# Kernel optimization log

Hardware: AMD Instinct MI355X
Metric: run time of the kernel (lower is better)

## Reference

```python
import jax, jax.numpy as jnp
import numpy as np

B, S, E = 2, 2048, 1024
H, KVH, D = 16, 4, 64
ROPE_BASE = 10000.0


def setup_inputs() -> dict:
    key = jax.random.key(0)
    ks = jax.random.split(key, 7)
    s = 0.02
    return {
        "query_inputs": jax.random.normal(ks[0], (B, S, E), jnp.float32),
        "key_inputs": jax.random.normal(ks[1], (B, S, E), jnp.float32),
        "value_inputs": jax.random.normal(ks[2], (B, S, E), jnp.float32),
        "attention_mask": jnp.ones((1, 1, S, S), dtype=bool),
        "Wq": jax.random.normal(ks[3], (E, H * D), jnp.float32) * s,
        "Wk": jax.random.normal(ks[4], (E, KVH * D), jnp.float32) * s,
        "Wv": jax.random.normal(ks[5], (E, KVH * D), jnp.float32) * s,
        "Wo": jax.random.normal(ks[6], (H * D, E), jnp.float32) * s,
    }


def _rotate_half(x):
    x1, x2 = jnp.split(x, 2, axis=-1)
    return jnp.concatenate((-x2, x1), axis=-1)


def _rope(k, q):
    # standard RoPE, rescaling_factor=None -> base 10000
    d = q.shape[-1]
    inv_freq = 1.0 / (ROPE_BASE ** (jnp.arange(0, d, 2, dtype=jnp.float32) / d))
    t = jnp.arange(q.shape[1], dtype=jnp.float32)
    freqs = jnp.einsum("i,j->ij", t, inv_freq)          # [S, d/2]
    emb = jnp.concatenate((freqs, freqs), axis=-1)       # [S, d]
    cos = jnp.cos(emb)[None, :, None, :]                 # [1, S, 1, d]
    sin = jnp.sin(emb)[None, :, None, :]
    apply = lambda x: x * cos + _rotate_half(x) * sin
    return apply(k), apply(q)


def reference(query_inputs, key_inputs, value_inputs, attention_mask, Wq, Wk, Wv, Wo):
    q = (query_inputs @ Wq).reshape(B, S, H, D)
    k = (key_inputs @ Wk).reshape(B, S, KVH, D)
    v = (value_inputs @ Wv).reshape(B, S, KVH, D)
    k, q = _rope(k, q)
    n_rep = H // KVH
    k = jnp.repeat(k, n_rep, axis=2)                     # [B, S, H, D]
    v = jnp.repeat(v, n_rep, axis=2)
    logits = jnp.einsum("bthd,bThd->bhtT", q, k) / jnp.sqrt(jnp.float32(D))
    logits = jnp.where(attention_mask, logits, jnp.float32(-1e30))
    w = jax.nn.softmax(logits, axis=-1)                  # [B, H, S, S]
    out = jnp.einsum("bhtT,bThd->bthd", w, v).reshape(B, S, H * D)
    return out @ Wo
```

## Files before the change

### kernel.cpp

```cpp
#include <hip/hip_runtime.h>
#include <hip/hip_bf16.h>
#include <math.h>

#define Bsz 2
#define Sseq 2048
#define Edim 1024
#define Hq 16
#define KVH 4
#define Dh 64

typedef __attribute__((ext_vector_type(2))) float f32x2;
typedef __attribute__((ext_vector_type(4))) float f32x4;
typedef __attribute__((ext_vector_type(16))) float f32x16;
typedef __attribute__((ext_vector_type(8))) short bf16x8;

__device__ inline unsigned short f2bf(float f) {
    union { float f; unsigned int u; } v; v.f = f;
    unsigned int u = v.u;
    u += 0x7FFFu + ((u >> 16) & 1u);
    return (unsigned short)(u >> 16);
}

__device__ inline float bf2f(unsigned short u) {
    union { unsigned int u; float f; } v; v.u = (unsigned int)u << 16;
    return v.f;
}

__device__ inline unsigned int cvt_pk_bf16(float a, float b) {
    unsigned int r;
    asm("v_cvt_pk_bf16_f32 %0, %1, %2" : "=v"(r) : "v"(a), "v"(b));
    return r;
}

__device__ inline f32x4 mfma16(bf16x8 a, bf16x8 b, f32x4 c) {
    return __builtin_amdgcn_mfma_f32_16x16x32_bf16(a, b, c, 0, 0, 0);
}

__device__ inline f32x16 mfma32(bf16x8 a, bf16x8 b, f32x16 c) {
    return __builtin_amdgcn_mfma_f32_32x32x16_bf16(a, b, c, 0, 0, 0);
}

__device__ inline void gload_lds16(const void* g, void* l) {
    __builtin_amdgcn_global_load_lds(
        (const __attribute__((address_space(1))) unsigned int*)g,
        (__attribute__((address_space(3))) unsigned int*)l, 16, 0, 0);
}

__global__ __launch_bounds__(256)
void prep(const float* __restrict__ Xq, const float* __restrict__ Xk,
          const float* __restrict__ Xv,
          const float* __restrict__ Wq, const float* __restrict__ Wk,
          const float* __restrict__ Wv, const float* __restrict__ Wo,
          unsigned short* __restrict__ Xq_b, unsigned short* __restrict__ Xk_b,
          unsigned short* __restrict__ Xv_b,
          unsigned short* __restrict__ Wq_t, unsigned short* __restrict__ Wk_t,
          unsigned short* __restrict__ Wv_t, unsigned short* __restrict__ Wo_t,
          float* __restrict__ tab) {
    int bid = blockIdx.x;
    if (bid < 256) {
        int idx = bid * 256 + threadIdx.x;
        int s = idx >> 5, j = idx & 31;
        double inv = pow(10000.0, -(double)(2 * j) / 64.0);
        double a = (double)s * inv;
        tab[idx * 2 + 0] = (float)cos(a);
        tab[idx * 2 + 1] = (float)sin(a);
        return;
    }
    bid -= 256;
    if (bid < 12288) {
        const float* X; unsigned short* Y;
        if (bid < 4096)      { X = Xq; Y = Xq_b; }
        else if (bid < 8192) { X = Xk; Y = Xk_b; bid -= 4096; }
        else                 { X = Xv; Y = Xv_b; bid -= 8192; }
        int i = bid * 256 + threadIdx.x;
        float4 v = ((const float4*)X)[i];
        ushort4 o;
        o.x = f2bf(v.x); o.y = f2bf(v.y); o.z = f2bf(v.z); o.w = f2bf(v.w);
        ((ushort4*)Y)[i] = o;
        return;
    }
    bid -= 12288;
    const float* W; unsigned short* Wt; int N; int local;
    if (bid < 1024)      { W = Wq; Wt = Wq_t; N = 1024; local = bid; }
    else if (bid < 1280) { W = Wk; Wt = Wk_t; N = 256;  local = bid - 1024; }
    else if (bid < 1536) { W = Wv; Wt = Wv_t; N = 256;  local = bid - 1280; }
    else                 { W = Wo; Wt = Wo_t; N = 1024; local = bid - 1536; }
    __shared__ float tile[32][33];
    int nb = N >> 5;
    int bn = (local % nb) * 32, bk = (local / nb) * 32;
    int tx = threadIdx.x & 31, ty = threadIdx.x >> 5;
    #pragma unroll
    for (int i = 0; i < 32; i += 8)
        tile[ty + i][tx] = W[(size_t)(bk + ty + i) * N + bn + tx];
    __syncthreads();
    #pragma unroll
    for (int i = 0; i < 32; i += 8)
        Wt[(size_t)(bn + ty + i) * 1024 + bk + tx] = f2bf(tile[tx][ty + i]);
}

__global__ __launch_bounds__(256)
void qkv_gemm(const unsigned short* __restrict__ Xq_b,
              const unsigned short* __restrict__ Xk_b,
              const unsigned short* __restrict__ Xv_b,
              const unsigned short* __restrict__ Wq_t,
              const unsigned short* __restrict__ Wk_t,
              const unsigned short* __restrict__ Wv_t,
              unsigned short* __restrict__ Qb,
              unsigned short* __restrict__ Kbf,
              unsigned short* __restrict__ Vt,
              const float* __restrict__ tab, float qscale) {
    __shared__ __attribute__((aligned(16))) unsigned short Alds[128 * 64];
    __shared__ __attribute__((aligned(16))) unsigned short Blds[64 * 64];

    int bid = blockIdx.x;
    const unsigned short *A, *Bt;
    unsigned short* C;
    int m0, n0, N, epi;
    float prescale;
    if (bid < 512) {
        A = Xq_b; Bt = Wq_t; C = Qb;
        m0 = (bid & 31) << 7; n0 = (bid >> 5) << 6; N = 1024; epi = 0; prescale = qscale;
    } else if (bid < 640) {
        int l = bid - 512;
        A = Xk_b; Bt = Wk_t; C = Kbf;
        m0 = (l & 31) << 7; n0 = (l >> 5) << 6; N = 256; epi = 0; prescale = 1.f;
    } else {
        int l = bid - 640;
        A = Xv_b; Bt = Wv_t; C = Vt;
        m0 = (l & 31) << 7; n0 = (l >> 5) << 6; N = 256; epi = 1; prescale = 1.f;
    }

    const int t = threadIdx.x;
    const int wid = t >> 6, lane = t & 63;
    const int l15 = lane & 15, l4 = lane >> 4;
    const int wm = wid * 32;

    f32x4 acc[2][4] = {};

    for (int k0 = 0; k0 < 1024; k0 += 64) {
        #pragma unroll
        for (int i = 0; i < 4; ++i) {
            int slot = t + 256 * i;
            int row = slot >> 3, ch = slot & 7;
            int g = ch ^ (row & 7);
            gload_lds16(A + (size_t)(m0 + row) * 1024 + k0 + g * 8, &Alds[slot * 8]);
        }
        #pragma unroll
        for (int i = 0; i < 2; ++i) {
            int slot = t + 256 * i;
            int row = slot >> 3, ch = slot & 7;
            int g = ch ^ (row & 7);
            gload_lds16(Bt + (size_t)(n0 + row) * 1024 + k0 + g * 8, &Blds[slot * 8]);
        }
        __syncthreads();
        __builtin_amdgcn_s_setprio(1);
        #pragma unroll
        for (int kc = 0; kc < 2; ++kc) {
            bf16x8 af[2], bfr[4];
            #pragma unroll
            for (int mt = 0; mt < 2; ++mt)
                af[mt] = *(const bf16x8*)&Alds[(wm + mt * 16 + l15) * 64 + (((kc * 4 + l4) ^ (l15 & 7)) * 8)];
            #pragma unroll
            for (int nt = 0; nt < 4; ++nt)
                bfr[nt] = *(const bf16x8*)&Blds[(nt * 16 + l15) * 64 + (((kc * 4 + l4) ^ (l15 & 7)) * 8)];
            #pragma unroll
            for (int mt = 0; mt < 2; ++mt)
                #pragma unroll
                for (int nt = 0; nt < 4; ++nt)
                    acc[mt][nt] = mfma16(af[mt], bfr[nt], acc[mt][nt]);
        }
        __builtin_amdgcn_s_setprio(0);
        __syncthreads();
    }

    if (epi == 0) {
        #pragma unroll
        for (int mt = 0; mt < 2; ++mt) {
            int rbase = m0 + wm + mt * 16 + 4 * l4;
            #pragma unroll
            for (int nt = 0; nt < 2; ++nt) {
                int col = n0 + nt * 16 + l15;
                int j = col & 31;
                #pragma unroll
                for (int r = 0; r < 4; ++r) {
                    int row = rbase + r;
                    int s = row & (Sseq - 1);
                    float c = tab[(s * 32 + j) * 2 + 0];
                    float sn = tab[(s * 32 + j) * 2 + 1];
                    float x1 = acc[mt][nt][r] * prescale;
                    float x2 = acc[mt][nt + 2][r] * prescale;
                    C[(size_t)row * N + col]      = f2bf(x1 * c - x2 * sn);
                    C[(size_t)row * N + col + 32] = f2bf(x2 * c + x1 * sn);
                }
            }
        }
    } else {
        #pragma unroll
        for (int mt = 0; mt < 2; ++mt)
            #pragma unroll
            for (int nt = 0; nt < 4; ++nt)
                #pragma unroll
                for (int r = 0; r < 4; ++r) {
                    int row = m0 + wm + mt * 16 + 4 * l4 + r;
                    int col = n0 + nt * 16 + l15;
                    int b = row >> 11, s = row & (Sseq - 1);
                    C[((size_t)(b * 256 + col) << 11) + s] = f2bf(acc[mt][nt][r]);
                }
    }
}

__global__ __launch_bounds__(256)
void wo_gemm(const unsigned short* __restrict__ A,
             const unsigned short* __restrict__ Bt,
             float* __restrict__ C) {
    __shared__ __attribute__((aligned(16))) unsigned short Alds[128 * 64];
    __shared__ __attribute__((aligned(16))) unsigned short Blds[64 * 64];
    const int t = threadIdx.x;
    const int wid = t >> 6, lane = t & 63;
    const int l15 = lane & 15, l4 = lane >> 4;
    const int m0 = blockIdx.x * 128, n0 = blockIdx.y * 64;
    const int wm = wid * 32;

    f32x4 acc[2][4] = {};

    for (int k0 = 0; k0 < 1024; k0 += 64) {
        #pragma unroll
        for (int i = 0; i < 4; ++i) {
            int slot = t + 256 * i;
            int row = slot >> 3, ch = slot & 7;
            int g = ch ^ (row & 7);
            gload_lds16(A + (size_t)(m0 + row) * 1024 + k0 + g * 8, &Alds[slot * 8]);
        }
        #pragma unroll
        for (int i = 0; i < 2; ++i) {
            int slot = t + 256 * i;
            int row = slot >> 3, ch = slot & 7;
            int g = ch ^ (row & 7);
            gload_lds16(Bt + (size_t)(n0 + row) * 1024 + k0 + g * 8, &Blds[slot * 8]);
        }
        __syncthreads();
        __builtin_amdgcn_s_setprio(1);
        #pragma unroll
        for (int kc = 0; kc < 2; ++kc) {
            bf16x8 af[2], bfr[4];
            #pragma unroll
            for (int mt = 0; mt < 2; ++mt)
                af[mt] = *(const bf16x8*)&Alds[(wm + mt * 16 + l15) * 64 + (((kc * 4 + l4) ^ (l15 & 7)) * 8)];
            #pragma unroll
            for (int nt = 0; nt < 4; ++nt)
                bfr[nt] = *(const bf16x8*)&Blds[(nt * 16 + l15) * 64 + (((kc * 4 + l4) ^ (l15 & 7)) * 8)];
            #pragma unroll
            for (int mt = 0; mt < 2; ++mt)
                #pragma unroll
                for (int nt = 0; nt < 4; ++nt)
                    acc[mt][nt] = mfma16(af[mt], bfr[nt], acc[mt][nt]);
        }
        __builtin_amdgcn_s_setprio(0);
        __syncthreads();
    }

    #pragma unroll
    for (int mt = 0; mt < 2; ++mt)
        #pragma unroll
        for (int nt = 0; nt < 4; ++nt)
            #pragma unroll
            for (int r = 0; r < 4; ++r)
                C[(size_t)(m0 + wm + mt * 16 + 4 * l4 + r) * 1024 + n0 + nt * 16 + l15]
                    = acc[mt][nt][r];
}

__global__ __launch_bounds__(256, 4)
void attn_split(const unsigned short* __restrict__ Q,
                const unsigned short* __restrict__ Kb,
                const unsigned short* __restrict__ Vt,
                unsigned short* __restrict__ Op,
                float* __restrict__ Lp) {
    __shared__ __attribute__((aligned(16))) unsigned short Klds[2][64 * 64];
    __shared__ __attribute__((aligned(16))) unsigned short Vlds[2][64 * 64];

    const int t = threadIdx.x, wid = t >> 6, lane = t & 63;
    const int l31 = lane & 31, hi = lane >> 5;
    const int q0 = blockIdx.x * 128;
    const int bh = blockIdx.y;
    const int half = blockIdx.z;
    const int b = bh >> 4, h = bh & 15, kvh = h >> 2;
    const int qb0 = (b << 11) + q0 + wid * 32;
    const int kh0 = half * 1024;

    bf16x8 qf[4];
    {
        const unsigned short* qp = Q + (size_t)(qb0 + l31) * 1024 + h * 64 + hi * 8;
        #pragma unroll
        for (int kc = 0; kc < 4; ++kc)
            qf[kc] = *(const bf16x8*)(qp + kc * 16);
    }

    const int r0 = t >> 3, c0 = t & 7;
    const int g0 = c0 ^ (r0 & 7);
    const int r1 = r0 + 32;
    const int g1 = c0 ^ (r1 & 7);
    const unsigned short* kp0 = Kb + (((size_t)((b << 11) + kh0 + r0)) << 8) + kvh * 64 + g0 * 8;
    const unsigned short* kp1 = Kb + (((size_t)((b << 11) + kh0 + r1)) << 8) + kvh * 64 + g1 * 8;
    const unsigned short* vp0 = Vt + (((size_t)((b * 4 + kvh) * 64 + r0)) << 11) + kh0 + g0 * 8;
    const unsigned short* vp1 = Vt + (((size_t)((b * 4 + kvh) * 64 + r1)) << 11) + kh0 + g1 * 8;

    f32x16 accO[2] = {};
    float lrow = 0.f;

    #define STAGE(buf)                                                    \
        do {                                                              \
            gload_lds16(kp0, &Klds[buf][t * 8]);                          \
            gload_lds16(kp1, &Klds[buf][(t + 256) * 8]);                  \
            gload_lds16(vp0, &Vlds[buf][t * 8]);                          \
            gload_lds16(vp1, &Vlds[buf][(t + 256) * 8]);                  \
            kp0 += 64 * 256; kp1 += 64 * 256; vp0 += 64; vp1 += 64;       \
        } while (0)

    STAGE(0);
    asm volatile("s_waitcnt vmcnt(0)");
    __syncthreads();

    int cur = 0;
    for (int kt = 0; kt < 16; ++kt) {
        if (kt + 1 < 16) STAGE(cur ^ 1);

        f32x16 sacc[2] = {};
        __builtin_amdgcn_s_setprio(1);
        #pragma unroll
        for (int kc = 0; kc < 4; ++kc) {
            #pragma unroll
            for (int kb = 0; kb < 2; ++kb) {
                int row = kb * 32 + l31;
                bf16x8 kf = *(const bf16x8*)
                    &Klds[cur][row * 64 + (((kc * 2 + hi) ^ (row & 7)) * 8)];
                sacc[kb] = mfma32(kf, qf[kc], sacc[kb]);
            }
        }
        __builtin_amdgcn_s_setprio(0);

        float pv[2][16];
        f32x2 rs2 = {0.f, 0.f};
        #pragma unroll
        for (int kb = 0; kb < 2; ++kb)
            #pragma unroll
            for (int r = 0; r < 16; r += 2) {
                float p0 = __builtin_amdgcn_exp2f(sacc[kb][r]);
                float p1 = __builtin_amdgcn_exp2f(sacc[kb][r + 1]);
                pv[kb][r] = p0;
                pv[kb][r + 1] = p1;
                rs2 += (f32x2){p0, p1};
            }
        float rs = rs2[0] + rs2[1];
        lrow += rs + __shfl_xor(rs, 32);

        bf16x8 pa[4];
        #pragma unroll
        for (int kb = 0; kb < 2; ++kb) {
            #pragma unroll
            for (int hf = 0; hf < 2; ++hf) {
                const float* p = &pv[kb][hf * 8];
                unsigned int u0 = cvt_pk_bf16(p[0], p[1]);
                unsigned int u1 = cvt_pk_bf16(p[2], p[3]);
                unsigned int u2 = cvt_pk_bf16(p[4], p[5]);
                unsigned int u3 = cvt_pk_bf16(p[6], p[7]);
                asm("v_permlane32_swap_b32 %0, %1" : "+v"(u0), "+v"(u2));
                asm("v_permlane32_swap_b32 %0, %1" : "+v"(u1), "+v"(u3));
                uint4 w; w.x = u0; w.y = u1; w.z = u2; w.w = u3;
                pa[kb * 2 + hf] = *(bf16x8*)&w;
            }
        }

        __builtin_amdgcn_s_setprio(1);
        #pragma unroll
        for (int kq = 0; kq < 4; ++kq) {
            #pragma unroll
            for (int db = 0; db < 2; ++db) {
                int row = db * 32 + l31;
                bf16x8 vf = *(const bf16x8*)
                    &Vlds[cur][row * 64 + (((kq * 2 + hi) ^ (row & 7)) * 8)];
                accO[db] = mfma32(pa[kq], vf, accO[db]);
            }
        }
        __builtin_amdgcn_s_setprio(0);

        asm volatile("s_waitcnt vmcnt(0)");
        __syncthreads();
        cur ^= 1;
    }
    #undef STAGE

    float linv = __builtin_amdgcn_rcpf(lrow);
    unsigned short* Oh = Op + (size_t)half * 4194304;
    #pragma unroll
    for (int r = 0; r < 16; ++r) {
        int q = (r & 3) + 8 * (r >> 2) + 4 * hi;
        float li = __shfl(linv, q);
        #pragma unroll
        for (int db = 0; db < 2; ++db)
            Oh[(size_t)(qb0 + q) * 1024 + h * 64 + db * 32 + l31] = f2bf(accO[db][r] * li);
    }
    if (hi == 0)
        Lp[half * 65536 + (bh << 11) + q0 + wid * 32 + l31] = lrow;
}

__global__ __launch_bounds__(256)
void combine(const unsigned short* __restrict__ Op, const float* __restrict__ Lp,
             unsigned short* __restrict__ AttO) {
    const int q = blockIdx.x, t = threadIdx.x;
    const int b = q >> 11, s = q & 2047, h = t >> 4;
    const int bh = (b << 4) | h;
    float l0 = Lp[(bh << 11) + s];
    float l1 = Lp[65536 + (bh << 11) + s];
    float w = __builtin_amdgcn_rcpf(l0 + l1);
    float w0 = l0 * w, w1 = l1 * w;
    size_t idx = (size_t)q * 1024 + t * 4;
    ushort4 a = *(const ushort4*)(Op + idx);
    ushort4 c = *(const ushort4*)(Op + 4194304 + idx);
    ushort4 o;
    o.x = f2bf(w0 * bf2f(a.x) + w1 * bf2f(c.x));
    o.y = f2bf(w0 * bf2f(a.y) + w1 * bf2f(c.y));
    o.z = f2bf(w0 * bf2f(a.z) + w1 * bf2f(c.z));
    o.w = f2bf(w0 * bf2f(a.w) + w1 * bf2f(c.w));
    *(ushort4*)(AttO + idx) = o;
}

extern "C" void kernel_launch(void* const* d_in, const int* in_sizes, int n_in,
                              void* d_out, int out_size, void* d_ws, size_t ws_size,
                              hipStream_t stream) {
    const float* Xq = (const float*)d_in[0];
    const float* Xk = (const float*)d_in[1];
    const float* Xv = (const float*)d_in[2];
    const float* Wq = (const float*)d_in[4];
    const float* Wk = (const float*)d_in[5];
    const float* Wv = (const float*)d_in[6];
    const float* Wo = (const float*)d_in[7];

    char* ws = (char*)d_ws;
    unsigned short* Xq_b = (unsigned short*)(ws + 0);
    unsigned short* Xk_b = (unsigned short*)(ws + 8388608);
    unsigned short* Xv_b = (unsigned short*)(ws + 16777216);
    unsigned short* Qb   = (unsigned short*)(ws + 25165824);
    unsigned short* Kbf  = (unsigned short*)(ws + 33554432);
    unsigned short* Vt   = (unsigned short*)(ws + 35651584);
    unsigned short* AttO = (unsigned short*)(ws + 37748736);
    unsigned short* Wq_t = (unsigned short*)(ws + 46137344);
    unsigned short* Wk_t = (unsigned short*)(ws + 48234496);
    unsigned short* Wv_t = (unsigned short*)(ws + 48758784);
    unsigned short* Wo_t = (unsigned short*)(ws + 49283072);
    float*          tab  = (float*)(ws + 51380224);
    unsigned short* Op   = (unsigned short*)(ws + 0);
    float*          Lp   = (float*)(ws + 16777216);

    prep<<<dim3(15104), 256, 0, stream>>>(Xq, Xk, Xv, Wq, Wk, Wv, Wo,
                                          Xq_b, Xk_b, Xv_b,
                                          Wq_t, Wk_t, Wv_t, Wo_t, tab);

    const float qscale = 0.125f * 1.44269504088896340736f;
    qkv_gemm<<<dim3(768), 256, 0, stream>>>(Xq_b, Xk_b, Xv_b, Wq_t, Wk_t, Wv_t,
                                            Qb, Kbf, Vt, tab, qscale);

    attn_split<<<dim3(16, 32, 2), 256, 0, stream>>>(Qb, Kbf, Vt, Op, Lp);
    combine<<<dim3(4096), 256, 0, stream>>>(Op, Lp, AttO);

    wo_gemm<<<dim3(32, 16), 256, 0, stream>>>(AttO, Wo_t, (float*)d_out);
}
```

Before: 104.3 us.

## Split attention KV range four ways with 32-key tiles

The attention kernel now splits each query block's key range into four parts of 512 keys instead of two of 1024, processing 32-key tiles per iteration with smaller LDS buffers. The grid doubles to raise occupancy and parallelism, and the combine kernel merges four partial outputs, with the fourth partial stored in the AttO buffer and Lp relocated. This trades more partial-output traffic and smaller MFMA work per sync for more concurrent blocks. It also risks aliasing, since the Lp slot moves onto the Wq_t region, which is presumably already consumed by then.

New measurement: 109.9 us. 1.05x slower.

```diff
diff --git a/kernel.cpp b/kernel.cpp
--- a/kernel.cpp
+++ b/kernel.cpp
@@ -9,7 +9,6 @@
 #define KVH 4
 #define Dh 64
 
-typedef __attribute__((ext_vector_type(2))) float f32x2;
 typedef __attribute__((ext_vector_type(4))) float f32x4;
 typedef __attribute__((ext_vector_type(16))) float f32x16;
 typedef __attribute__((ext_vector_type(8))) short bf16x8;
@@ -274,18 +273,19 @@
                 const unsigned short* __restrict__ Kb,
                 const unsigned short* __restrict__ Vt,
                 unsigned short* __restrict__ Op,
+                unsigned short* __restrict__ Op3,
                 float* __restrict__ Lp) {
-    __shared__ __attribute__((aligned(16))) unsigned short Klds[2][64 * 64];
-    __shared__ __attribute__((aligned(16))) unsigned short Vlds[2][64 * 64];
+    __shared__ __attribute__((aligned(16))) unsigned short Klds[2][32 * 64];
+    __shared__ __attribute__((aligned(16))) unsigned short Vlds[2][64 * 32];
 
     const int t = threadIdx.x, wid = t >> 6, lane = t & 63;
     const int l31 = lane & 31, hi = lane >> 5;
     const int q0 = blockIdx.x * 128;
     const int bh = blockIdx.y;
-    const int half = blockIdx.z;
+    const int split = blockIdx.z;
     const int b = bh >> 4, h = bh & 15, kvh = h >> 2;
     const int qb0 = (b << 11) + q0 + wid * 32;
-    const int kh0 = half * 1024;
+    const int kh0 = split * 512;
 
     bf16x8 qf[4];
     {
@@ -295,25 +295,21 @@
             qf[kc] = *(const bf16x8*)(qp + kc * 16);
     }
 
-    const int r0 = t >> 3, c0 = t & 7;
-    const int g0 = c0 ^ (r0 & 7);
-    const int r1 = r0 + 32;
-    const int g1 = c0 ^ (r1 & 7);
-    const unsigned short* kp0 = Kb + (((size_t)((b << 11) + kh0 + r0)) << 8) + kvh * 64 + g0 * 8;
-    const unsigned short* kp1 = Kb + (((size_t)((b << 11) + kh0 + r1)) << 8) + kvh * 64 + g1 * 8;
-    const unsigned short* vp0 = Vt + (((size_t)((b * 4 + kvh) * 64 + r0)) << 11) + kh0 + g0 * 8;
-    const unsigned short* vp1 = Vt + (((size_t)((b * 4 + kvh) * 64 + r1)) << 11) + kh0 + g1 * 8;
+    const int kr = t >> 3, kc8 = t & 7;
+    const int kg = kc8 ^ (kr & 7);
+    const int vr = t >> 2, vc = t & 3;
+    const int vg = vc ^ (vr & 3);
+    const unsigned short* kp = Kb + (((size_t)((b << 11) + kh0 + kr)) << 8) + kvh * 64 + kg * 8;
+    const unsigned short* vp = Vt + (((size_t)((b * 4 + kvh) * 64 + vr)) << 11) + kh0 + vg * 8;
 
     f32x16 accO[2] = {};
     float lrow = 0.f;
 
     #define STAGE(buf)                                                    \
         do {                                                              \
-            gload_lds16(kp0, &Klds[buf][t * 8]);                          \
-            gload_lds16(kp1, &Klds[buf][(t + 256) * 8]);                  \
-            gload_lds16(vp0, &Vlds[buf][t * 8]);                          \
-            gload_lds16(vp1, &Vlds[buf][(t + 256) * 8]);                  \
-            kp0 += 64 * 256; kp1 += 64 * 256; vp0 += 64; vp1 += 64;       \
+            gload_lds16(kp, &Klds[buf][t * 8]);                           \
+            gload_lds16(vp, &Vlds[buf][t * 8]);                           \
+            kp += 32 * 256; vp += 32;                                     \
         } while (0)
 
     STAGE(0);
@@ -324,60 +320,48 @@
     for (int kt = 0; kt < 16; ++kt) {
         if (kt + 1 < 16) STAGE(cur ^ 1);
 
-        f32x16 sacc[2] = {};
+        f32x16 sacc = {};
         __builtin_amdgcn_s_setprio(1);
         #pragma unroll
         for (int kc = 0; kc < 4; ++kc) {
-            #pragma unroll
-            for (int kb = 0; kb < 2; ++kb) {
-                int row = kb * 32 + l31;
-                bf16x8 kf = *(const bf16x8*)
-                    &Klds[cur][row * 64 + (((kc * 2 + hi) ^ (row & 7)) * 8)];
-                sacc[kb] = mfma32(kf, qf[kc], sacc[kb]);
-            }
+            bf16x8 kf = *(const bf16x8*)
+                &Klds[cur][l31 * 64 + (((kc * 2 + hi) ^ (l31 & 7)) * 8)];
+            sacc = mfma32(kf, qf[kc], sacc);
         }
         __builtin_amdgcn_s_setprio(0);
 
-        float pv[2][16];
-        f32x2 rs2 = {0.f, 0.f};
-        #pragma unroll
-        for (int kb = 0; kb < 2; ++kb)
-            #pragma unroll
-            for (int r = 0; r < 16; r += 2) {
-                float p0 = __builtin_amdgcn_exp2f(sacc[kb][r]);
-                float p1 = __builtin_amdgcn_exp2f(sacc[kb][r + 1]);
-                pv[kb][r] = p0;
-                pv[kb][r + 1] = p1;
-                rs2 += (f32x2){p0, p1};
-            }
-        float rs = rs2[0] + rs2[1];
+        float pv[16];
+        float rs = 0.f;
+        #pragma unroll
+        for (int r = 0; r < 16; ++r) {
+            float p = __builtin_amdgcn_exp2f(sacc[r]);
+            pv[r] = p;
+            rs += p;
+        }
         lrow += rs + __shfl_xor(rs, 32);
 
-        bf16x8 pa[4];
-        #pragma unroll
-        for (int kb = 0; kb < 2; ++kb) {
-            #pragma unroll
-            for (int hf = 0; hf < 2; ++hf) {
-                const float* p = &pv[kb][hf * 8];
-                unsigned int u0 = cvt_pk_bf16(p[0], p[1]);
-                unsigned int u1 = cvt_pk_bf16(p[2], p[3]);
-                unsigned int u2 = cvt_pk_bf16(p[4], p[5]);
-                unsigned int u3 = cvt_pk_bf16(p[6], p[7]);
-                asm("v_permlane32_swap_b32 %0, %1" : "+v"(u0), "+v"(u2));
-                asm("v_permlane32_swap_b32 %0, %1" : "+v"(u1), "+v"(u3));
-                uint4 w; w.x = u0; w.y = u1; w.z = u2; w.w = u3;
-                pa[kb * 2 + hf] = *(bf16x8*)&w;
-            }
+        bf16x8 pa[2];
+        #pragma unroll
+        for (int hf = 0; hf < 2; ++hf) {
+            const float* p = &pv[hf * 8];
+            unsigned int u0 = cvt_pk_bf16(p[0], p[1]);
+            unsigned int u1 = cvt_pk_bf16(p[2], p[3]);
+            unsigned int u2 = cvt_pk_bf16(p[4], p[5]);
+            unsigned int u3 = cvt_pk_bf16(p[6], p[7]);
+            asm("v_permlane32_swap_b32 %0, %1" : "+v"(u0), "+v"(u2));
+            asm("v_permlane32_swap_b32 %0, %1" : "+v"(u1), "+v"(u3));
+            uint4 w; w.x = u0; w.y = u1; w.z = u2; w.w = u3;
+            pa[hf] = *(bf16x8*)&w;
         }
 
         __builtin_amdgcn_s_setprio(1);
         #pragma unroll
-        for (int kq = 0; kq < 4; ++kq) {
+        for (int kq = 0; kq < 2; ++kq) {
             #pragma unroll
             for (int db = 0; db < 2; ++db) {
                 int row = db * 32 + l31;
                 bf16x8 vf = *(const bf16x8*)
-                    &Vlds[cur][row * 64 + (((kq * 2 + hi) ^ (row & 7)) * 8)];
+                    &Vlds[cur][row * 32 + (((kq * 2 + hi) ^ (row & 3)) * 8)];
                 accO[db] = mfma32(pa[kq], vf, accO[db]);
             }
         }
@@ -390,7 +374,7 @@
     #undef STAGE
 
     float linv = __builtin_amdgcn_rcpf(lrow);
-    unsigned short* Oh = Op + (size_t)half * 4194304;
+    unsigned short* Oh = (split == 3) ? Op3 : (Op + (size_t)split * 4194304);
     #pragma unroll
     for (int r = 0; r < 16; ++r) {
         int q = (r & 3) + 8 * (r >> 2) + 4 * hi;
@@ -400,7 +384,7 @@
             Oh[(size_t)(qb0 + q) * 1024 + h * 64 + db * 32 + l31] = f2bf(accO[db][r] * li);
     }
     if (hi == 0)
-        Lp[half * 65536 + (bh << 11) + q0 + wid * 32 + l31] = lrow;
+        Lp[split * 65536 + (bh << 11) + q0 + wid * 32 + l31] = lrow;
 }
 
 __global__ __launch_bounds__(256)
@@ -411,16 +395,20 @@
     const int bh = (b << 4) | h;
     float l0 = Lp[(bh << 11) + s];
     float l1 = Lp[65536 + (bh << 11) + s];
-    float w = __builtin_amdgcn_rcpf(l0 + l1);
-    float w0 = l0 * w, w1 = l1 * w;
+    float l2 = Lp[131072 + (bh << 11) + s];
+    float l3 = Lp[196608 + (bh << 11) + s];
+    float w = __builtin_amdgcn_rcpf(l0 + l1 + l2 + l3);
+    float w0 = l0 * w, w1 = l1 * w, w2 = l2 * w, w3 = l3 * w;
     size_t idx = (size_t)q * 1024 + t * 4;
     ushort4 a = *(const ushort4*)(Op + idx);
     ushort4 c = *(const ushort4*)(Op + 4194304 + idx);
+    ushort4 d = *(const ushort4*)(Op + 8388608 + idx);
+    ushort4 e = *(const ushort4*)(AttO + idx);
     ushort4 o;
-    o.x = f2bf(w0 * bf2f(a.x) + w1 * bf2f(c.x));
-    o.y = f2bf(w0 * bf2f(a.y) + w1 * bf2f(c.y));
-    o.z = f2bf(w0 * bf2f(a.z) + w1 * bf2f(c.z));
-    o.w = f2bf(w0 * bf2f(a.w) + w1 * bf2f(c.w));
+    o.x = f2bf(w0 * bf2f(a.x) + w1 * bf2f(c.x) + w2 * bf2f(d.x) + w3 * bf2f(e.x));
+    o.y = f2bf(w0 * bf2f(a.y) + w1 * bf2f(c.y) + w2 * bf2f(d.y) + w3 * bf2f(e.y));
+    o.z = f2bf(w0 * bf2f(a.z) + w1 * bf2f(c.z) + w2 * bf2f(d.z) + w3 * bf2f(e.z));
+    o.w = f2bf(w0 * bf2f(a.w) + w1 * bf2f(c.w) + w2 * bf2f(d.w) + w3 * bf2f(e.w));
     *(ushort4*)(AttO + idx) = o;
 }
 
@@ -449,7 +437,7 @@
     unsigned short* Wo_t = (unsigned short*)(ws + 49283072);
     float*          tab  = (float*)(ws + 51380224);
     unsigned short* Op   = (unsigned short*)(ws + 0);
-    float*          Lp   = (float*)(ws + 16777216);
+    float*          Lp   = (float*)(ws + 46137344);
 
     prep<<<dim3(15104), 256, 0, stream>>>(Xq, Xk, Xv, Wq, Wk, Wv, Wo,
                                           Xq_b, Xk_b, Xv_b,
@@ -459,7 +447,7 @@
     qkv_gemm<<<dim3(768), 256, 0, stream>>>(Xq_b, Xk_b, Xv_b, Wq_t, Wk_t, Wv_t,
                                             Qb, Kbf, Vt, tab, qscale);
 
-    attn_split<<<dim3(16, 32, 2), 256, 0, stream>>>(Qb, Kbf, Vt, Op, Lp);
+    attn_split<<<dim3(16, 32, 4), 256, 0, stream>>>(Qb, Kbf, Vt, Op, AttO, Lp);
     combine<<<dim3(4096), 256, 0, stream>>>(Op, Lp, AttO);
 
     wo_gemm<<<dim3(32, 16), 256, 0, stream>>>(AttO, Wo_t, (float*)d_out);
```

## Load K/V fragments directly from global memory instead of LDS double buffering

Applied to the files above, without the earlier changes.

The attention kernel no longer stages K and V tiles into double-buffered shared memory. Each lane now reads its MFMA operand fragments straight from global memory, relying on L1/L2 caching across the four waves that share a KV head. This removes the LDS traffic and the per-iteration barriers, and adds a 2x unroll so loads can be issued early. The risk is that redundant global loads and exposed latency outweigh the saved synchronization. The exp results are also written back into the score accumulator in place of a separate array.

Result: slower. 179.2 us (+71.8%).

```diff
diff --git a/kernel.cpp b/kernel.cpp
--- a/kernel.cpp
+++ b/kernel.cpp
@@ -9,7 +9,6 @@
 #define KVH 4
 #define Dh 64
 
-typedef __attribute__((ext_vector_type(2))) float f32x2;
 typedef __attribute__((ext_vector_type(4))) float f32x4;
 typedef __attribute__((ext_vector_type(16))) float f32x16;
 typedef __attribute__((ext_vector_type(8))) short bf16x8;
@@ -275,9 +274,6 @@
                 const unsigned short* __restrict__ Vt,
                 unsigned short* __restrict__ Op,
                 float* __restrict__ Lp) {
-    __shared__ __attribute__((aligned(16))) unsigned short Klds[2][64 * 64];
-    __shared__ __attribute__((aligned(16))) unsigned short Vlds[2][64 * 64];
-
     const int t = threadIdx.x, wid = t >> 6, lane = t & 63;
     const int l31 = lane & 31, hi = lane >> 5;
     const int q0 = blockIdx.x * 128;
@@ -295,34 +291,16 @@
             qf[kc] = *(const bf16x8*)(qp + kc * 16);
     }
 
-    const int r0 = t >> 3, c0 = t & 7;
-    const int g0 = c0 ^ (r0 & 7);
-    const int r1 = r0 + 32;
-    const int g1 = c0 ^ (r1 & 7);
-    const unsigned short* kp0 = Kb + (((size_t)((b << 11) + kh0 + r0)) << 8) + kvh * 64 + g0 * 8;
-    const unsigned short* kp1 = Kb + (((size_t)((b << 11) + kh0 + r1)) << 8) + kvh * 64 + g1 * 8;
-    const unsigned short* vp0 = Vt + (((size_t)((b * 4 + kvh) * 64 + r0)) << 11) + kh0 + g0 * 8;
-    const unsigned short* vp1 = Vt + (((size_t)((b * 4 + kvh) * 64 + r1)) << 11) + kh0 + g1 * 8;
+    const unsigned short* kpl = Kb + (((size_t)((b << 11) + kh0 + l31)) << 8) + kvh * 64 + hi * 8;
+    const unsigned short* vpl = Vt + (((size_t)((b * 4 + kvh) * 64 + l31)) << 11) + kh0 + hi * 8;
 
     f32x16 accO[2] = {};
     float lrow = 0.f;
 
-    #define STAGE(buf)                                                    \
-        do {                                                              \
-            gload_lds16(kp0, &Klds[buf][t * 8]);                          \
-            gload_lds16(kp1, &Klds[buf][(t + 256) * 8]);                  \
-            gload_lds16(vp0, &Vlds[buf][t * 8]);                          \
-            gload_lds16(vp1, &Vlds[buf][(t + 256) * 8]);                  \
-            kp0 += 64 * 256; kp1 += 64 * 256; vp0 += 64; vp1 += 64;       \
-        } while (0)
-
-    STAGE(0);
-    asm volatile("s_waitcnt vmcnt(0)");
-    __syncthreads();
-
-    int cur = 0;
+    #pragma unroll 2
     for (int kt = 0; kt < 16; ++kt) {
-        if (kt + 1 < 16) STAGE(cur ^ 1);
+        const unsigned short* kp = kpl + (size_t)kt * 64 * 256;
+        const unsigned short* vp = vpl + kt * 64;
 
         f32x16 sacc[2] = {};
         __builtin_amdgcn_s_setprio(1);
@@ -330,27 +308,21 @@
         for (int kc = 0; kc < 4; ++kc) {
             #pragma unroll
             for (int kb = 0; kb < 2; ++kb) {
-                int row = kb * 32 + l31;
-                bf16x8 kf = *(const bf16x8*)
-                    &Klds[cur][row * 64 + (((kc * 2 + hi) ^ (row & 7)) * 8)];
+                bf16x8 kf = *(const bf16x8*)(kp + (size_t)kb * 32 * 256 + kc * 16);
                 sacc[kb] = mfma32(kf, qf[kc], sacc[kb]);
             }
         }
         __builtin_amdgcn_s_setprio(0);
 
-        float pv[2][16];
-        f32x2 rs2 = {0.f, 0.f};
+        float rs = 0.f;
         #pragma unroll
         for (int kb = 0; kb < 2; ++kb)
             #pragma unroll
-            for (int r = 0; r < 16; r += 2) {
-                float p0 = __builtin_amdgcn_exp2f(sacc[kb][r]);
-                float p1 = __builtin_amdgcn_exp2f(sacc[kb][r + 1]);
-                pv[kb][r] = p0;
-                pv[kb][r + 1] = p1;
-                rs2 += (f32x2){p0, p1};
+            for (int r = 0; r < 16; ++r) {
+                float p = __builtin_amdgcn_exp2f(sacc[kb][r]);
+                sacc[kb][r] = p;
+                rs += p;
             }
-        float rs = rs2[0] + rs2[1];
         lrow += rs + __shfl_xor(rs, 32);
 
         bf16x8 pa[4];
@@ -358,7 +330,7 @@
         for (int kb = 0; kb < 2; ++kb) {
             #pragma unroll
             for (int hf = 0; hf < 2; ++hf) {
-                const float* p = &pv[kb][hf * 8];
+                const float* p = (const float*)&sacc[kb] + hf * 8;
                 unsigned int u0 = cvt_pk_bf16(p[0], p[1]);
                 unsigned int u1 = cvt_pk_bf16(p[2], p[3]);
                 unsigned int u2 = cvt_pk_bf16(p[4], p[5]);
@@ -375,19 +347,12 @@
         for (int kq = 0; kq < 4; ++kq) {
             #pragma unroll
             for (int db = 0; db < 2; ++db) {
-                int row = db * 32 + l31;
-                bf16x8 vf = *(const bf16x8*)
-                    &Vlds[cur][row * 64 + (((kq * 2 + hi) ^ (row & 7)) * 8)];
+                bf16x8 vf = *(const bf16x8*)(vp + (size_t)db * 32 * 2048 + kq * 16);
                 accO[db] = mfma32(pa[kq], vf, accO[db]);
             }
         }
         __builtin_amdgcn_s_setprio(0);
-
-        asm volatile("s_waitcnt vmcnt(0)");
-        __syncthreads();
-        cur ^= 1;
-    }
-    #undef STAGE
+    }
 
     float linv = __builtin_amdgcn_rcpf(lrow);
     unsigned short* Oh = Op + (size_t)half * 4194304;
```
